# Performance work log

Measured on AMD Instinct MI355X. Metric: run time of the kernel, lower is better.

The kernel has to match this reference:

```python
import jax, jax.numpy as jnp
import numpy as np

K = 5        # kernel_size per dim
DIM = 3      # pseudo-coordinate dim
KTOT = K ** DIM   # 125 kernel weight matrices
S = 2 ** DIM      # 8 basis products for degree-1 open B-spline
KNN = 3


def spline_basis(ea):
    """Degree-1 open B-spline basis. ea: [E, DIM] in [0,1).
    Returns basis [E, S] and kernel weight indices wi [E, S]."""
    v = ea * (K - 1)
    b = jnp.floor(v)
    f = v - b                      # fractional part, grads flow here
    bi = b.astype(jnp.int32)
    bases, idxs = [], []
    for c in range(S):             # static loop over 2^DIM corner combos
        bs = jnp.ones(ea.shape[0], ea.dtype)
        wi = jnp.zeros(ea.shape[0], jnp.int32)
        for d in range(DIM):
            bit = (c >> d) & 1
            bs = bs * (f[:, d] if bit else 1.0 - f[:, d])
            wi = wi + jnp.clip(bi[:, d] + bit, 0, K - 1) * (K ** d)
        bases.append(bs)
        idxs.append(wi)
    return jnp.stack(bases, 1), jnp.stack(idxs, 1)


def spline_conv(x, src, dst, basis, wi, W, Wroot, bias):
    """SplineConv with aggr='mean', root weight and bias (PyG defaults)."""
    N, Cin = x.shape
    E = src.shape[0]
    xs = x[src]                                   # [E, Cin] gather
    vals = xs[:, None, :] * basis[:, :, None]     # [E, S, Cin]
    seg = (dst[:, None] * KTOT + wi).reshape(-1)  # bucket by (dst node, kernel)
    A = jax.ops.segment_sum(vals.reshape(-1, Cin), seg,
                            num_segments=N * KTOT).reshape(N, KTOT, Cin)
    out = jnp.einsum('nki,kio->no', A, W)         # apply kernel bank once
    deg = jax.ops.segment_sum(jnp.ones(E, x.dtype), dst, num_segments=N)
    out = out / jnp.maximum(deg, 1.0)[:, None]    # mean aggregation
    return out + x @ Wroot + bias


def knn_interpolate(x, pos_x, pos_y, batch_x, batch_y, k):
    """PyG knn_interpolate: inverse-squared-distance weighted k-NN average."""
    off = 1e5  # separate batches in coordinate space
    px = pos_x + batch_x[:, None].astype(pos_x.dtype) * off
    py = pos_y + batch_y[:, None].astype(pos_y.dtype) * off
    d2 = (jnp.sum(py ** 2, 1)[:, None] + jnp.sum(px ** 2, 1)[None, :]
          - 2.0 * (py @ px.T))                    # [Ny, Nx]
    negd, idx = jax.lax.top_k(-d2, k)             # k nearest
    w = 1.0 / jnp.maximum(-negd, 1e-16)           # [Ny, k]
    return (w[:, :, None] * x[idx]).sum(1) / w.sum(1)[:, None]


def setup_inputs() -> dict:
    key = jax.random.key(0)
    ks = jax.random.split(key, 12)
    N, E, Ny, C = 8192, 131072, 16384, 64
    return {
        'x': jax.random.normal(ks[0], (N, C), jnp.float32),
        'edge_index': jax.random.randint(ks[1], (2, E), 0, N, jnp.int32),
        'edge_attr': jax.random.uniform(ks[2], (E, DIM), jnp.float32),
        'pos_x': jax.random.normal(ks[3], (N, 3), jnp.float32),
        'batch_x': jnp.zeros((N,), jnp.int32),
        'pos_y': jax.random.normal(ks[4], (Ny, 3), jnp.float32),
        'batch_y': jnp.zeros((Ny,), jnp.int32),
        'Wa': jax.random.normal(ks[5], (KTOT, C, C), jnp.float32) * 0.05,
        'roota': jax.random.normal(ks[6], (C, C), jnp.float32) * 0.05,
        'biasa': jnp.zeros((C,), jnp.float32),
        'Wb': jax.random.normal(ks[7], (KTOT, C, C), jnp.float32) * 0.05,
        'rootb': jax.random.normal(ks[8], (C, C), jnp.float32) * 0.05,
        'biasb': jnp.zeros((C,), jnp.float32),
    }


def reference(x, edge_index, edge_attr, pos_x, batch_x, pos_y, batch_y,
              Wa, roota, biasa, Wb, rootb, biasb):
    src, dst = edge_index[0], edge_index[1]
    basis, wi = spline_basis(edge_attr)
    h = jax.nn.elu(spline_conv(x, src, dst, basis, wi, Wa, roota, biasa))
    h = jax.nn.elu(spline_conv(h, src, dst, basis, wi, Wb, rootb, biasb))
    return knn_interpolate(h, pos_x, pos_y, batch_x, batch_y, KNN)
```

## Files before the change

kernel.cpp:

```cpp
#include <hip/hip_runtime.h>
#include <hip/hip_bf16.h>
#include <math.h>

#define CDIV(a,b) (((a)+(b)-1)/(b))
#define WPCV 8
#define KCH 32

typedef __attribute__((ext_vector_type(8))) short bf16x8;
typedef __attribute__((ext_vector_type(4))) float f32x4;

__device__ __forceinline__ float elu_f(float x){ return x > 0.f ? x : expm1f(x); }
__device__ __forceinline__ unsigned short f2bf(float x){
    __hip_bfloat16 h = __float2bfloat16(x);
    union { __hip_bfloat16 b; unsigned short u; } cv; cv.b = h; return cv.u;
}
__device__ __forceinline__ float bf2f(unsigned short u){
    unsigned int ui = ((unsigned int)u) << 16;
    union { unsigned int u; float f; } cv; cv.u = ui; return cv.f;
}

__global__ void k_basis_px(const float* __restrict__ ea, const int* __restrict__ dst,
                        float* __restrict__ basis, int* __restrict__ cellid,
                        int* __restrict__ cellcnt, int* __restrict__ deg,
                        int* __restrict__ rank, int E, int EB,
                        const float* __restrict__ posx, const int* __restrict__ bx,
                        float4* __restrict__ px4, int N)
{
    const int tid = threadIdx.x;
    if ((int)blockIdx.x >= EB) {
        int n = ((int)blockIdx.x - EB)*256 + tid;
        if (n < N) {
            float off = (float)bx[n] * 1e5f;
            float a = posx[n*3+0]+off, b = posx[n*3+1]+off, c = posx[n*3+2]+off;
            px4[n] = make_float4(a, b, c, a*a + b*b + c*c);
        }
        return;
    }
    __shared__ int hist[64];
    if (tid < 64) hist[tid] = 0;
    __syncthreads();
    int e = blockIdx.x * blockDim.x + tid;
    if (e < E) {
        float f[3]; int bi[3];
        #pragma unroll
        for (int d = 0; d < 3; d++) {
            float v = ea[e*3+d] * 4.f;
            float b = floorf(v);
            f[d] = v - b;
            int bb = (int)b; bb = bb < 0 ? 0 : (bb > 3 ? 3 : bb);
            bi[d] = bb;
        }
        int cell = bi[0] + 4*bi[1] + 16*bi[2];
        cellid[e] = cell;
        atomicAdd(&hist[cell], 1);
        rank[e] = atomicAdd(deg + dst[e], 1);
        float bs[8];
        #pragma unroll
        for (int c = 0; c < 8; c++) {
            float b = 1.f;
            #pragma unroll
            for (int d = 0; d < 3; d++)
                b *= ((c>>d)&1) ? f[d] : (1.f - f[d]);
            bs[c] = b;
        }
        float4* bw = (float4*)(basis + (size_t)e*8);
        bw[0] = make_float4(bs[0],bs[1],bs[2],bs[3]);
        bw[1] = make_float4(bs[4],bs[5],bs[6],bs[7]);
    }
    __syncthreads();
    if (tid < 64 && hist[tid]) atomicAdd(cellcnt + tid, hist[tid]);
}

__global__ __launch_bounds__(1024) void k_degscan(const int* __restrict__ deg,
                        int* __restrict__ csr, float* __restrict__ invdeg, int N,
                        const int* __restrict__ cellcnt, int* __restrict__ cellstart,
                        int* __restrict__ cellfill)
{
    __shared__ int buf[2][1024];
    const int t = threadIdx.x;
    if (t < 64) {
        int v = cellcnt[t];
        int s = v;
        #pragma unroll
        for (int off = 1; off < 64; off <<= 1) {
            int o = __shfl_up(s, off, 64);
            if (t >= off) s += o;
        }
        cellstart[t] = s - v; cellfill[t] = s - v;
        if (t == 63) cellstart[64] = s;
    }
    const int base = t*8;
    int loc[8]; int s = 0;
    #pragma unroll
    for (int j = 0; j < 8; j++) {
        loc[j] = s;
        int d = (base+j < N) ? deg[base+j] : 0;
        if (base+j < N) invdeg[base+j] = 1.f / fmaxf((float)d, 1.f);
        s += d;
    }
    buf[0][t] = s; __syncthreads();
    int pb = 0;
    for (int off = 1; off < 1024; off <<= 1) {
        int v = buf[pb][t];
        if (t >= off) v += buf[pb][t-off];
        buf[pb^1][t] = v; __syncthreads(); pb ^= 1;
    }
    int excl = buf[pb][t] - s;
    #pragma unroll
    for (int j = 0; j < 8; j++)
        if (base+j < N) csr[base+j] = excl + loc[j];
    if (t == 0) csr[N] = buf[pb][1023];
}

__global__ __launch_bounds__(256) void k_pack(
    const int* __restrict__ cellid, int* __restrict__ fill, int* __restrict__ elist,
    const int* __restrict__ dst, const int* __restrict__ rank,
    const int* __restrict__ csr, int* __restrict__ eord, int E, int SB,
    const float* __restrict__ Wa, const float* __restrict__ Wb,
    unsigned short* __restrict__ WTa, unsigned short* __restrict__ WTb)
{
    __shared__ float shbuf[64*65];
    const int tid = threadIdx.x;
    const int bid = blockIdx.x;
    if (bid < SB) {
        int* hist = (int*)shbuf;
        int* bas  = hist + 64;
        if (tid < 64) hist[tid] = 0;
        __syncthreads();
        int e = bid * 256 + tid;
        int cell = 0, loc = 0;
        bool act = e < E;
        if (act) { cell = cellid[e]; loc = atomicAdd(&hist[cell], 1); }
        __syncthreads();
        if (tid < 64) bas[tid] = hist[tid] ? atomicAdd(fill + tid, hist[tid]) : 0;
        __syncthreads();
        if (act) elist[bas[cell] + loc] = e;
    } else if (bid < 2*SB) {
        int e = (bid - SB) * 256 + tid;
        if (e < E) eord[csr[dst[e]] + rank[e]] = e;
    } else {
        int b = bid - 2*SB;
        float (*ws65)[65] = (float(*)[65])shbuf;
        const float* Wsrc = (b < 125) ? (Wa + (size_t)b*4096) : (Wb + (size_t)(b-125)*4096);
        unsigned short* Wdst = (b < 125) ? (WTa + (size_t)b*4096) : (WTb + (size_t)(b-125)*4096);
        #pragma unroll
        for (int j = 0; j < 16; j++) {
            int idx = j*256 + tid;
            ws65[idx>>6][idx&63] = Wsrc[idx];
        }
        __syncthreads();
        #pragma unroll
        for (int j = 0; j < 16; j++) {
            int idx = j*256 + tid;
            int o = idx>>6, i = idx&63;
            Wdst[idx] = f2bf(ws65[i][o]);
        }
    }
}

__global__ __launch_bounds__(256) void k_conv(
    const float* __restrict__ xin, const unsigned short* __restrict__ WT,
    const int* __restrict__ elist, const int* __restrict__ cellstart,
    const float* __restrict__ basis, const int* __restrict__ src,
    unsigned short* __restrict__ ye)
{
    __shared__ unsigned short wt[8][64][64];
    __shared__ unsigned short xb[64][64];
    __shared__ float bts[8][64];
    __shared__ int eids[64];

    const int cell = blockIdx.x / WPCV;
    const int sub  = blockIdx.x % WPCV;
    const int tid  = threadIdx.x;
    const int w    = tid >> 6;
    const int lane = tid & 63;
    const int eh   = w >> 1;
    const int oh   = w & 1;
    const int l15  = lane & 15;
    const int kgrp = lane >> 4;
    const int swz  = lane & 7;

    int kc[8];
    {
        int b0 = cell & 3, b1 = (cell >> 2) & 3, b2 = (cell >> 4) & 3;
        #pragma unroll
        for (int c = 0; c < 8; c++)
            kc[c] = (b0 + (c&1)) + 5*(b1 + ((c>>1)&1)) + 25*(b2 + ((c>>2)&1));
    }

    #pragma unroll
    for (int j = 0; j < 16; j++) {
        int cj  = j >> 1;
        int off = ((j & 1) << 8) + tid;
        int row = off >> 3, colc = off & 7;
        bf16x8 v = ((const bf16x8*)(WT + (size_t)kc[cj]*4096))[off];
        *(bf16x8*)&wt[cj][row][(colc ^ (row & 7)) << 3] = v;
    }

    const int s0 = cellstart[cell], s1 = cellstart[cell+1];
    const int se = tid >> 2, sm = tid & 3;

    for (int base = s0 + sub*64; base < s1; base += WPCV*64) {
        int ne = s1 - base; ne = ne > 64 ? 64 : ne;
        __syncthreads();
        if (se < ne) {
            int eid = elist[base + se];
            int sn  = src[eid];
            const float4* xr = (const float4*)(xin + (size_t)sn*64);
            unsigned short tmp[16];
            #pragma unroll
            for (int j = 0; j < 4; j++) {
                float4 v = xr[sm*4 + j];
                tmp[j*4+0] = f2bf(v.x); tmp[j*4+1] = f2bf(v.y);
                tmp[j*4+2] = f2bf(v.z); tmp[j*4+3] = f2bf(v.w);
            }
            int c0 = (sm*2)     ^ (se & 7);
            int c1 = (sm*2 + 1) ^ (se & 7);
            *(bf16x8*)&xb[se][c0 << 3] = *(bf16x8*)&tmp[0];
            *(bf16x8*)&xb[se][c1 << 3] = *(bf16x8*)&tmp[8];
            if (sm == 0) {
                const float4* br = (const float4*)(basis + (size_t)eid*8);
                float4 bA = br[0], bB = br[1];
                bts[0][se]=bA.x; bts[1][se]=bA.y; bts[2][se]=bA.z; bts[3][se]=bA.w;
                bts[4][se]=bB.x; bts[5][se]=bB.y; bts[6][se]=bB.z; bts[7][se]=bB.w;
                eids[se] = eid;
            }
        } else if (sm == 0) {
            eids[se] = -1;
        }
        __syncthreads();

        bf16x8 a[2][2];
        #pragma unroll
        for (int me = 0; me < 2; me++) {
            int arow = eh*32 + me*16 + l15;
            #pragma unroll
            for (int kh = 0; kh < 2; kh++)
                a[me][kh] = *(const bf16x8*)&xb[arow][((kh*4 + kgrp) ^ swz) << 3];
        }

        f32x4 y[2][2] = {{{0,0,0,0},{0,0,0,0}},{{0,0,0,0},{0,0,0,0}}};
        #pragma unroll
        for (int c = 0; c < 8; c++) {
            float4 bv[2];
            bv[0] = *(const float4*)&bts[c][eh*32 +      (kgrp << 2)];
            bv[1] = *(const float4*)&bts[c][eh*32 + 16 + (kgrp << 2)];
            bf16x8 bfr[2][2];
            #pragma unroll
            for (int nb = 0; nb < 2; nb++) {
                int brow = oh*32 + nb*16 + l15;
                #pragma unroll
                for (int kh = 0; kh < 2; kh++)
                    bfr[nb][kh] = *(const bf16x8*)&wt[c][brow][((kh*4 + kgrp) ^ swz) << 3];
            }
            #pragma unroll
            for (int me = 0; me < 2; me++) {
                #pragma unroll
                for (int nb = 0; nb < 2; nb++) {
                    f32x4 t = {0.f, 0.f, 0.f, 0.f};
                    t = __builtin_amdgcn_mfma_f32_16x16x32_bf16(a[me][0], bfr[nb][0], t, 0, 0, 0);
                    t = __builtin_amdgcn_mfma_f32_16x16x32_bf16(a[me][1], bfr[nb][1], t, 0, 0, 0);
                    y[me][nb][0] = fmaf(bv[me].x, t[0], y[me][nb][0]);
                    y[me][nb][1] = fmaf(bv[me].y, t[1], y[me][nb][1]);
                    y[me][nb][2] = fmaf(bv[me].z, t[2], y[me][nb][2]);
                    y[me][nb][3] = fmaf(bv[me].w, t[3], y[me][nb][3]);
                }
            }
        }
        #pragma unroll
        for (int me = 0; me < 2; me++) {
            #pragma unroll
            for (int r = 0; r < 4; r++) {
                int el  = eh*32 + me*16 + (kgrp << 2) + r;
                int eid = eids[el];
                if (eid >= 0) {
                    unsigned short* yp = ye + (size_t)eid*64 + oh*32 + l15;
                    yp[0]  = f2bf(y[me][0][r]);
                    yp[16] = f2bf(y[me][1][r]);
                }
            }
        }
    }
}

__global__ __launch_bounds__(256) void k_gather(
    const unsigned short* __restrict__ ye, const int* __restrict__ eord,
    const int* __restrict__ csr, const float* __restrict__ xin,
    const float* __restrict__ root, const float* __restrict__ bias,
    const float* __restrict__ invdeg, float* __restrict__ hout, int N)
{
    const int w = threadIdx.x >> 6, lane = threadIdx.x & 63;
    const int n = blockIdx.x*4 + w;
    if (n >= N) return;
    const int s0 = csr[n], s1 = csr[n+1];
    float acc0 = 0.f, acc1 = 0.f;
    int j = s0;
    for (; j + 1 < s1; j += 2) {
        int e0 = eord[j], e1 = eord[j+1];
        acc0 += bf2f(ye[(size_t)e0*64 + lane]);
        acc1 += bf2f(ye[(size_t)e1*64 + lane]);
    }
    if (j < s1) acc0 += bf2f(ye[(size_t)eord[j]*64 + lane]);
    float acc = (acc0 + acc1) * invdeg[n];
    float xv = xin[(size_t)n*64 + lane];
    float rt = bias[lane];
    #pragma unroll 8
    for (int i = 0; i < 64; i++)
        rt = fmaf(__shfl(xv, i, 64), root[i*64 + lane], rt);
    hout[(size_t)n*64 + lane] = elu_f(acc + rt);
}

__global__ __launch_bounds__(512) void k_knn_part(
    const float4* __restrict__ px4, const float* __restrict__ posy,
    const int* __restrict__ by, float* __restrict__ pd, int* __restrict__ pi,
    int N, int Ny)
{
    const int qb  = (blockIdx.x / KCH) * 512;
    const int ch  = blockIdx.x % KCH;
    const int NC  = N / KCH;
    const int tid = threadIdx.x;
    const int q = qb + tid;
    float off = (float)by[q] * 1e5f;
    float qa = posy[q*3+0]+off, qbv = posy[q*3+1]+off, qc = posy[q*3+2]+off;
    float sy = qa*qa + qbv*qbv + qc*qc;
    float qa2 = -2.f*qa, qb2 = -2.f*qbv, qc2 = -2.f*qc;

    const float4* __restrict__ pts = px4 + (size_t)ch * NC;
    const int gbase = ch * NC;

    float d0 = 3.4e38f, d1 = 3.4e38f, d2s = 3.4e38f;
    int   i0 = 0x7fffffff, i1 = 0x7fffffff, i2 = 0x7fffffff;
    #pragma unroll 16
    for (int p = 0; p < NC; p++) {
        float4 pt = pts[p];
        float u  = fmaf(qa2, pt.x, fmaf(qb2, pt.y, fmaf(qc2, pt.z, sy + pt.w)));
        int   gi = gbase + p;
        bool c0 = u < d0, c1 = u < d1, c2 = u < d2s;
        float nd0 = fminf(d0, u);
        float nd1 = __builtin_amdgcn_fmed3f(d0, u, d1);
        float nd2 = __builtin_amdgcn_fmed3f(u, d1, d2s);
        i2 = c1 ? i1 : (c2 ? gi : i2);
        i1 = c0 ? i0 : (c1 ? gi : i1);
        i0 = c0 ? gi : i0;
        d0 = nd0; d1 = nd1; d2s = nd2;
    }
    size_t ob = ((size_t)ch*Ny + q)*3;
    pd[ob+0]=d0; pd[ob+1]=d1; pd[ob+2]=d2s;
    pi[ob+0]=i0; pi[ob+1]=i1; pi[ob+2]=i2;
}

__global__ __launch_bounds__(256) void k_knn_merge(
    const float* __restrict__ pd, const int* __restrict__ pi,
    const float* __restrict__ h2, float* __restrict__ out, int Ny)
{
    const int w = threadIdx.x >> 6, lane = threadIdx.x & 63;
    const int q = blockIdx.x*4 + w;
    float a0 = 3.4e38f, a1 = 3.4e38f, a2 = 3.4e38f;
    int   b0 = 0x7fffffff, b1 = 0x7fffffff, b2 = 0x7fffffff;
    if (lane < KCH) {
        size_t base = ((size_t)lane*Ny + q)*3;
        a0 = pd[base+0]; a1 = pd[base+1]; a2 = pd[base+2];
        b0 = pi[base+0]; b1 = pi[base+1]; b2 = pi[base+2];
    }
    float rd[3]; int ri[3];
    #pragma unroll
    for (int j = 0; j < 3; j++) {
        float md = a0; int mi = b0;
        #pragma unroll
        for (int s = 1; s < 64; s <<= 1) {
            float od = __shfl_xor(md, s, 64);
            int   oi = __shfl_xor(mi, s, 64);
            if (od < md || (od == md && oi < mi)) { md = od; mi = oi; }
        }
        rd[j] = md; ri[j] = mi;
        if (b0 == mi) { a0=a1; b0=b1; a1=a2; b1=b2; a2=3.4e38f; b2=0x7fffffff; }
    }
    float w0 = 1.f/fmaxf(rd[0], 1e-16f);
    float w1 = 1.f/fmaxf(rd[1], 1e-16f);
    float w2 = 1.f/fmaxf(rd[2], 1e-16f);
    float ws = w0 + w1 + w2;
    float v = w0*h2[(size_t)ri[0]*64+lane] + w1*h2[(size_t)ri[1]*64+lane]
            + w2*h2[(size_t)ri[2]*64+lane];
    out[(size_t)q*64+lane] = v / ws;
}

extern "C" void kernel_launch(void* const* d_in, const int* in_sizes, int n_in,
                              void* d_out, int out_size, void* d_ws, size_t ws_size,
                              hipStream_t stream)
{
    const float* x     = (const float*)d_in[0];
    const int*   ei    = (const int*)d_in[1];
    const float* ea    = (const float*)d_in[2];
    const float* posx  = (const float*)d_in[3];
    const int*   bx    = (const int*)d_in[4];
    const float* posy  = (const float*)d_in[5];
    const int*   by    = (const int*)d_in[6];
    const float* Wa    = (const float*)d_in[7];
    const float* roota = (const float*)d_in[8];
    const float* biasa = (const float*)d_in[9];
    const float* Wb    = (const float*)d_in[10];
    const float* rootb = (const float*)d_in[11];
    const float* biasb = (const float*)d_in[12];

    const int N  = in_sizes[0] / 64;
    const int E  = in_sizes[1] / 2;
    const int Ny = in_sizes[5] / 3;
    const int* srcp = ei;
    const int* dstp = ei + E;

    char* ws = (char*)d_ws;
    size_t off = 0;
    auto alloc = [&](size_t bytes) { void* p = ws + off; off += (bytes + 255) & ~255ull; return p; };
    float*  basis    = (float*)alloc((size_t)E*8*4);
    int*    cellid   = (int*)  alloc((size_t)E*4);
    int*    rank     = (int*)  alloc((size_t)E*4);
    int*    elist    = (int*)  alloc((size_t)E*4);
    int*    eord     = (int*)  alloc((size_t)E*4);
    int*    deg      = (int*)  alloc((size_t)N*4);
    int*    cellcnt  = (int*)  alloc(64*4);
    int*    csr      = (int*)  alloc((size_t)(N+1)*4);
    float*  invdeg   = (float*)alloc((size_t)N*4);
    int*    cellstart= (int*)  alloc(65*4);
    int*    cellfill = (int*)  alloc(64*4);
    float*  h1       = (float*)alloc((size_t)N*64*4);
    float*  h2       = (float*)alloc((size_t)N*64*4);
    float4* px4      = (float4*)alloc((size_t)N*16);
    unsigned short* WTa = (unsigned short*)alloc((size_t)125*4096*2);
    unsigned short* WTb = (unsigned short*)alloc((size_t)125*4096*2);
    unsigned short* ye  = (unsigned short*)alloc((size_t)E*64*2);
    float* pd = (float*)ye;
    int*   pi = (int*)((char*)ye + ((size_t)8<<20));
    (void)ws_size; (void)n_in; (void)out_size;

    const int EB = CDIV(E,256);
    const int PB = CDIV(N,256);

    hipMemsetAsync(deg, 0, (size_t)N*4 + 256, stream);

    k_basis_px<<<EB+PB, 256, 0, stream>>>(ea, dstp, basis, cellid, cellcnt, deg, rank,
                                          E, EB, posx, bx, px4, N);
    k_degscan <<<1, 1024, 0, stream>>>(deg, csr, invdeg, N, cellcnt, cellstart, cellfill);
    k_pack    <<<2*EB + 250, 256, 0, stream>>>(cellid, cellfill, elist, dstp, rank,
                                               csr, eord, E, EB, Wa, Wb, WTa, WTb);

    k_conv  <<<64*WPCV, 256, 0, stream>>>(x, WTa, elist, cellstart, basis, srcp, ye);
    k_gather<<<CDIV(N,4), 256, 0, stream>>>(ye, eord, csr, x, roota, biasa, invdeg, h1, N);

    k_conv  <<<64*WPCV, 256, 0, stream>>>(h1, WTb, elist, cellstart, basis, srcp, ye);
    k_gather<<<CDIV(N,4), 256, 0, stream>>>(ye, eord, csr, h1, rootb, biasb, invdeg, h2, N);

    k_knn_part <<<(Ny/512)*KCH, 512, 0, stream>>>(px4, posy, by, pd, pi, N, Ny);
    k_knn_merge<<<Ny/4, 256, 0, stream>>>(pd, pi, h2, (float*)d_out, Ny);
}
```

Baseline: 182.5 us.

## Scatter conv outputs in destination-sorted order and vectorize gather reduction

The conv kernel now writes each edge's output row directly at its CSR destination position, so the gather kernel reads a contiguous range of rows instead of chasing an edge-order index. Gather lanes load 8 bf16 values at a time across 8 edges in parallel and reduce them with cross-lane shuffles through shared memory. The knn partial kernel also moves from 512-thread to 256-thread blocks. In exchange, conv stores become more scattered, and gather adds shuffle work plus a shared-memory round trip.

```diff
diff --git a/kernel.cpp b/kernel.cpp
--- a/kernel.cpp
+++ b/kernel.cpp
@@ -115,7 +115,7 @@
 __global__ __launch_bounds__(256) void k_pack(
     const int* __restrict__ cellid, int* __restrict__ fill, int* __restrict__ elist,
     const int* __restrict__ dst, const int* __restrict__ rank,
-    const int* __restrict__ csr, int* __restrict__ eord, int E, int SB,
+    const int* __restrict__ csr, int* __restrict__ dstpos, int E, int SB,
     const float* __restrict__ Wa, const float* __restrict__ Wb,
     unsigned short* __restrict__ WTa, unsigned short* __restrict__ WTb)
 {
@@ -137,7 +137,7 @@
         if (act) elist[bas[cell] + loc] = e;
     } else if (bid < 2*SB) {
         int e = (bid - SB) * 256 + tid;
-        if (e < E) eord[csr[dst[e]] + rank[e]] = e;
+        if (e < E) dstpos[e] = csr[dst[e]] + rank[e];
     } else {
         int b = bid - 2*SB;
         float (*ws65)[65] = (float(*)[65])shbuf;
@@ -162,12 +162,12 @@
     const float* __restrict__ xin, const unsigned short* __restrict__ WT,
     const int* __restrict__ elist, const int* __restrict__ cellstart,
     const float* __restrict__ basis, const int* __restrict__ src,
-    unsigned short* __restrict__ ye)
+    const int* __restrict__ dstpos, unsigned short* __restrict__ ye)
 {
     __shared__ unsigned short wt[8][64][64];
     __shared__ unsigned short xb[64][64];
     __shared__ float bts[8][64];
-    __shared__ int eids[64];
+    __shared__ int dpos[64];
 
     const int cell = blockIdx.x / WPCV;
     const int sub  = blockIdx.x % WPCV;
@@ -223,10 +223,10 @@
                 float4 bA = br[0], bB = br[1];
                 bts[0][se]=bA.x; bts[1][se]=bA.y; bts[2][se]=bA.z; bts[3][se]=bA.w;
                 bts[4][se]=bB.x; bts[5][se]=bB.y; bts[6][se]=bB.z; bts[7][se]=bB.w;
-                eids[se] = eid;
+                dpos[se] = dstpos[eid];
             }
         } else if (sm == 0) {
-            eids[se] = -1;
+            dpos[se] = -1;
         }
         __syncthreads();
 
@@ -271,10 +271,10 @@
         for (int me = 0; me < 2; me++) {
             #pragma unroll
             for (int r = 0; r < 4; r++) {
-                int el  = eh*32 + me*16 + (kgrp << 2) + r;
-                int eid = eids[el];
-                if (eid >= 0) {
-                    unsigned short* yp = ye + (size_t)eid*64 + oh*32 + l15;
+                int el = eh*32 + me*16 + (kgrp << 2) + r;
+                int dp = dpos[el];
+                if (dp >= 0) {
+                    unsigned short* yp = ye + (size_t)dp*64 + oh*32 + l15;
                     yp[0]  = f2bf(y[me][0][r]);
                     yp[16] = f2bf(y[me][1][r]);
                 }
@@ -284,38 +284,53 @@
 }
 
 __global__ __launch_bounds__(256) void k_gather(
-    const unsigned short* __restrict__ ye, const int* __restrict__ eord,
-    const int* __restrict__ csr, const float* __restrict__ xin,
-    const float* __restrict__ root, const float* __restrict__ bias,
-    const float* __restrict__ invdeg, float* __restrict__ hout, int N)
-{
+    const unsigned short* __restrict__ ye, const int* __restrict__ csr,
+    const float* __restrict__ xin, const float* __restrict__ root,
+    const float* __restrict__ bias, const float* __restrict__ invdeg,
+    float* __restrict__ hout, int N)
+{
+    __shared__ float sh[4][64];
     const int w = threadIdx.x >> 6, lane = threadIdx.x & 63;
     const int n = blockIdx.x*4 + w;
     if (n >= N) return;
     const int s0 = csr[n], s1 = csr[n+1];
-    float acc0 = 0.f, acc1 = 0.f;
-    int j = s0;
-    for (; j + 1 < s1; j += 2) {
-        int e0 = eord[j], e1 = eord[j+1];
-        acc0 += bf2f(ye[(size_t)e0*64 + lane]);
-        acc1 += bf2f(ye[(size_t)e1*64 + lane]);
-    }
-    if (j < s1) acc0 += bf2f(ye[(size_t)eord[j]*64 + lane]);
-    float acc = (acc0 + acc1) * invdeg[n];
+    const int j8 = lane >> 3, c8 = lane & 7;
+    float acc[8] = {};
+    for (int base = s0; base < s1; base += 8) {
+        int ei = base + j8;
+        if (ei < s1) {
+            bf16x8 v = *(const bf16x8*)(ye + (size_t)ei*64 + c8*8);
+            #pragma unroll
+            for (int k = 0; k < 8; k++)
+                acc[k] += bf2f((unsigned short)v[k]);
+        }
+    }
+    #pragma unroll
+    for (int m = 8; m <= 32; m <<= 1) {
+        #pragma unroll
+        for (int k = 0; k < 8; k++)
+            acc[k] += __shfl_xor(acc[k], m, 64);
+    }
+    if (j8 == 0) {
+        #pragma unroll
+        for (int k = 0; k < 8; k++) sh[w][c8*8+k] = acc[k];
+    }
+    float aggr = sh[w][lane];
+    float av = aggr * invdeg[n];
     float xv = xin[(size_t)n*64 + lane];
     float rt = bias[lane];
     #pragma unroll 8
     for (int i = 0; i < 64; i++)
         rt = fmaf(__shfl(xv, i, 64), root[i*64 + lane], rt);
-    hout[(size_t)n*64 + lane] = elu_f(acc + rt);
-}
-
-__global__ __launch_bounds__(512) void k_knn_part(
+    hout[(size_t)n*64 + lane] = elu_f(av + rt);
+}
+
+__global__ __launch_bounds__(256) void k_knn_part(
     const float4* __restrict__ px4, const float* __restrict__ posy,
     const int* __restrict__ by, float* __restrict__ pd, int* __restrict__ pi,
     int N, int Ny)
 {
-    const int qb  = (blockIdx.x / KCH) * 512;
+    const int qb  = (blockIdx.x / KCH) * 256;
     const int ch  = blockIdx.x % KCH;
     const int NC  = N / KCH;
     const int tid = threadIdx.x;
@@ -415,7 +430,7 @@
     int*    cellid   = (int*)  alloc((size_t)E*4);
     int*    rank     = (int*)  alloc((size_t)E*4);
     int*    elist    = (int*)  alloc((size_t)E*4);
-    int*    eord     = (int*)  alloc((size_t)E*4);
+    int*    dstpos   = (int*)  alloc((size_t)E*4);
     int*    deg      = (int*)  alloc((size_t)N*4);
     int*    cellcnt  = (int*)  alloc(64*4);
     int*    csr      = (int*)  alloc((size_t)(N+1)*4);
@@ -441,14 +456,14 @@
                                           E, EB, posx, bx, px4, N);
     k_degscan <<<1, 1024, 0, stream>>>(deg, csr, invdeg, N, cellcnt, cellstart, cellfill);
     k_pack    <<<2*EB + 250, 256, 0, stream>>>(cellid, cellfill, elist, dstp, rank,
-                                               csr, eord, E, EB, Wa, Wb, WTa, WTb);
-
-    k_conv  <<<64*WPCV, 256, 0, stream>>>(x, WTa, elist, cellstart, basis, srcp, ye);
-    k_gather<<<CDIV(N,4), 256, 0, stream>>>(ye, eord, csr, x, roota, biasa, invdeg, h1, N);
-
-    k_conv  <<<64*WPCV, 256, 0, stream>>>(h1, WTb, elist, cellstart, basis, srcp, ye);
-    k_gather<<<CDIV(N,4), 256, 0, stream>>>(ye, eord, csr, h1, rootb, biasb, invdeg, h2, N);
-
-    k_knn_part <<<(Ny/512)*KCH, 512, 0, stream>>>(px4, posy, by, pd, pi, N, Ny);
+                                               csr, dstpos, E, EB, Wa, Wb, WTa, WTb);
+
+    k_conv  <<<64*WPCV, 256, 0, stream>>>(x, WTa, elist, cellstart, basis, srcp, dstpos, ye);
+    k_gather<<<CDIV(N,4), 256, 0, stream>>>(ye, csr, x, roota, biasa, invdeg, h1, N);
+
+    k_conv  <<<64*WPCV, 256, 0, stream>>>(h1, WTb, elist, cellstart, basis, srcp, dstpos, ye);
+    k_gather<<<CDIV(N,4), 256, 0, stream>>>(ye, csr, h1, rootb, biasb, invdeg, h2, N);
+
+    k_knn_part <<<(Ny/256)*KCH, 256, 0, stream>>>(px4, posy, by, pd, pi, N, Ny);
     k_knn_merge<<<Ny/4, 256, 0, stream>>>(pd, pi, h2, (float*)d_out, Ny);
 }
```

New measurement: 178.1 us. 1.02x faster.
